# Performance work log

Hardware: AMD Instinct MI355X
Metric: run time of the kernel (lower is better)

The kernel has to match this reference:

```python
import jax, jax.numpy as jnp
import numpy as np

N_EMBD = 1024
HEAD_SIZE = 128
B, T = 8, 4096


def setup_inputs() -> dict:
    key = jax.random.key(0)
    ks = jax.random.split(key, 7)
    s = 1.0 / np.sqrt(N_EMBD)
    return {
        "x": jax.random.normal(ks[0], (B, T, N_EMBD), dtype=jnp.float32),
        "Wq": jax.random.uniform(ks[1], (N_EMBD, HEAD_SIZE), jnp.float32, -s, s),
        "bq": jax.random.uniform(ks[2], (HEAD_SIZE,), jnp.float32, -s, s),
        "Wk": jax.random.uniform(ks[3], (N_EMBD, HEAD_SIZE), jnp.float32, -s, s),
        "bk": jax.random.uniform(ks[4], (HEAD_SIZE,), jnp.float32, -s, s),
        "Wv": jax.random.uniform(ks[5], (N_EMBD, HEAD_SIZE), jnp.float32, -s, s),
        "bv": jax.random.uniform(ks[6], (HEAD_SIZE,), jnp.float32, -s, s),
    }


def reference(x, Wq, bq, Wk, bk, Wv, bv):
    # q,k,v: [B,T,H]
    q = x @ Wq + bq
    k = x @ Wk + bk
    v = x @ Wv + bv
    scale = HEAD_SIZE ** -0.5
    att = jnp.einsum("bth,bsh->bts", q, k) * scale  # [B,T,T]
    t = x.shape[1]
    causal = jnp.tril(jnp.ones((t, t), dtype=bool))
    att = jnp.where(causal, att, -jnp.inf)
    att = jax.nn.softmax(att, axis=-1)
    # dropout with p=0.0 is identity (eval-mode equivalent)
    out = jnp.einsum("bts,bsh->bth", att, v)  # [B,T,H]
    return out
```

## Files before the change

### kernel.cpp

```cpp
#include <hip/hip_runtime.h>
#include <hip/hip_bf16.h>
#include <stdint.h>

#define BATCH 8
#define SEQ   4096
#define EMB   1024
#define HD    128
#define NROWS 32768

typedef __attribute__((ext_vector_type(8))) short short8;
typedef __attribute__((ext_vector_type(4))) float f32x4;

__device__ inline unsigned short f2bf(float f) {
    union { float f; unsigned int u; } c; c.f = f;
    unsigned int u = c.u;
    unsigned int r = (u + 0x7fffu + ((u >> 16) & 1u)) >> 16;
    return (unsigned short)r;
}
__device__ inline float bf2f(unsigned short u) {
    union { unsigned int i; float f; } c; c.i = ((unsigned int)u) << 16; return c.f;
}
__device__ inline unsigned int pkbf(float a, float b) {
    __hip_bfloat162 h = __float22bfloat162_rn(make_float2(a, b));
    union { __hip_bfloat162 h; unsigned int u; } c; c.h = h; return c.u;
}

#define GLDS16(gp, lp) __builtin_amdgcn_global_load_lds( \
    (const __attribute__((address_space(1))) void*)(gp), \
    (__attribute__((address_space(3))) void*)(lp), 16, 0, 0)

__global__ __launch_bounds__(256) void prep_kernel(
    const float* __restrict__ Wq, const float* __restrict__ bq,
    const float* __restrict__ Wk, const float* __restrict__ bk,
    const float* __restrict__ Wv, const float* __restrict__ bv,
    unsigned short* __restrict__ wt, float* __restrict__ biasc)
{
    const int n = blockIdx.x;
    const int sel = n >> 7, h = n & 127;
    const float* W = (sel == 0) ? Wq : (sel == 1) ? Wk : Wv;
    const int tid = threadIdx.x;
    const int k0 = tid * 4;
    union { unsigned short us[4]; uint2 v; } pk;
#pragma unroll
    for (int u = 0; u < 4; ++u) pk.us[u] = f2bf(W[(size_t)(k0 + u) * HD + h]);
    *(uint2*)&wt[(size_t)n * EMB + k0] = pk.v;
    if (tid == 0) {
        const float* bp = (sel == 0) ? bq : (sel == 1) ? bk : bv;
        biasc[n] = bp[h];
    }
}

__global__ __launch_bounds__(768, 3) void gemm_qkv(
    const float* __restrict__ x, const unsigned short* __restrict__ wt,
    const float* __restrict__ biasc,
    unsigned short* __restrict__ q, unsigned short* __restrict__ kOut,
    unsigned short* __restrict__ vt)
{
    const int m0  = blockIdx.x * 128;
    const int tid = threadIdx.x;
    const int wave = tid >> 6, lane = tid & 63;
    const int quad = lane >> 4, l15 = lane & 15;
    const int wm = (wave >= 6) ? 1 : 0;
    const int wn = wave - wm * 6;

    __shared__ __align__(16) unsigned short As[2][128][40];
    __shared__ __align__(16) unsigned short Bs[2][12288];

    f32x4 acc[4][4];
#pragma unroll
    for (int i = 0; i < 4; ++i)
#pragma unroll
        for (int j = 0; j < 4; ++j) acc[i][j] = (f32x4){0.f, 0.f, 0.f, 0.f};

    const int aactive = (tid < 512);
    const int arow = tid >> 3, akc = (tid & 7) * 4;
    float4 aR0, aR1;

#define LOAD_A(kt)                                                          \
    if (aactive) {                                                          \
        aR0 = *(const float4*)(x + (size_t)(m0 + arow) * EMB + (kt) * 32 + akc);        \
        aR1 = *(const float4*)(x + (size_t)(m0 + arow + 64) * EMB + (kt) * 32 + akc);   \
    }
#define WRITE_A(buf)                                                        \
    if (aactive) {                                                          \
        union { unsigned short us[4]; uint2 v; } p0, p1;                    \
        p0.us[0] = f2bf(aR0.x); p0.us[1] = f2bf(aR0.y);                     \
        p0.us[2] = f2bf(aR0.z); p0.us[3] = f2bf(aR0.w);                     \
        *(uint2*)&As[buf][arow][akc] = p0.v;                                \
        p1.us[0] = f2bf(aR1.x); p1.us[1] = f2bf(aR1.y);                     \
        p1.us[2] = f2bf(aR1.z); p1.us[3] = f2bf(aR1.w);                     \
        *(uint2*)&As[buf][arow + 64][akc] = p1.v;                           \
    }
#define STAGE_B(kt, buf)                                                    \
    {                                                                       \
        _Pragma("unroll")                                                   \
        for (int g = 0; g < 2; ++g) {                                       \
            int s0 = (g * 12 + wave) * 64;                                  \
            int s  = s0 + lane;                                             \
            int n  = s >> 2, c = (s & 3) ^ (n & 3);                         \
            GLDS16(wt + (size_t)n * EMB + (kt) * 32 + c * 8,                \
                   &Bs[buf][s0 * 8]);                                       \
        }                                                                   \
    }

    LOAD_A(0); STAGE_B(0, 0); WRITE_A(0);
    int cur = 0;

    for (int kt = 0; kt < 32; ++kt) {
        __syncthreads();
        if (kt < 31) { LOAD_A(kt + 1); STAGE_B(kt + 1, cur ^ 1); }
        short8 af[4], bw[4];
#pragma unroll
        for (int mj = 0; mj < 4; ++mj)
            af[mj] = *(const short8*)&As[cur][wm * 64 + mj * 16 + l15][quad * 8];
#pragma unroll
        for (int ni = 0; ni < 4; ++ni) {
            int n = wn * 64 + ni * 16 + l15;
            bw[ni] = *(const short8*)&Bs[cur][n * 32 + ((quad ^ (n & 3)) << 3)];
        }
#pragma unroll
        for (int ni = 0; ni < 4; ++ni)
#pragma unroll
            for (int mj = 0; mj < 4; ++mj)
                acc[ni][mj] = __builtin_amdgcn_mfma_f32_16x16x32_bf16(
                    bw[ni], af[mj], acc[ni][mj], 0, 0, 0);
        if (kt < 31) WRITE_A(cur ^ 1);
        cur ^= 1;
    }

    const float qscale = 0.08838834764831845f * 1.4426950408889634f;
    const int bb = m0 >> 12;
    const int t0 = m0 & 4095;
    const int mrow0 = m0 + wm * 64;
    const int tl0   = t0 + wm * 64;
#pragma unroll
    for (int ni = 0; ni < 4; ++ni) {
        int colbase = wn * 64 + ni * 16;
        int sel = colbase >> 7;
        int c0 = colbase + quad * 4;
        float4 bv4 = *(const float4*)&biasc[c0];
#pragma unroll
        for (int mj = 0; mj < 4; ++mj) {
            int m = mrow0 + mj * 16 + l15;
            if (sel == 0) {
                union { unsigned short us[4]; uint2 v; } pk;
#pragma unroll
                for (int j = 0; j < 4; ++j)
                    pk.us[j] = f2bf((acc[ni][mj][j] + ((const float*)&bv4)[j]) * qscale);
                *(uint2*)&q[(size_t)m * HD + (c0 & 127)] = pk.v;
            } else if (sel == 1) {
                union { unsigned short us[4]; uint2 v; } pk;
#pragma unroll
                for (int j = 0; j < 4; ++j)
                    pk.us[j] = f2bf(acc[ni][mj][j] + ((const float*)&bv4)[j]);
                *(uint2*)&kOut[(size_t)m * HD + (c0 & 127)] = pk.v;
            } else {
#pragma unroll
                for (int j = 0; j < 4; ++j) {
                    int h = (c0 & 127) + j;
                    vt[((size_t)(bb * 128 + h)) * SEQ + tl0 + mj * 16 + l15] =
                        f2bf(acc[ni][mj][j] + ((const float*)&bv4)[j]);
                }
            }
        }
    }
#undef LOAD_A
#undef WRITE_A
#undef STAGE_B
}

__global__ __launch_bounds__(256, 2) void attn_kernel(
    const unsigned short* __restrict__ q, const unsigned short* __restrict__ k,
    const unsigned short* __restrict__ vt, float* __restrict__ outA,
    unsigned short* __restrict__ Oh, float2* __restrict__ ml)
{
    const int rank = blockIdx.x;
    int qt, parity;
    if (rank < 256) { parity = 0; qt = 31 - (rank >> 3); }
    else            { parity = 1; qt = (rank - 256) >> 3; }
    const int b = rank & 7;
    const int tid  = threadIdx.x;
    const int wave = tid >> 6, lane = tid & 63;
    const int quad = lane >> 4, l15 = lane & 15;
    const int qrow0 = qt * 128 + wave * 32;
    const size_t qbase = (size_t)b * SEQ;
    const size_t vbase = (size_t)b * HD * SEQ;

    __shared__ __align__(16) unsigned short Ks[2][8192];
    __shared__ __align__(16) unsigned short Vs[2][8192];

#define STAGE_KV(kt_, buf_)                                                  \
    {                                                                        \
        _Pragma("unroll")                                                    \
        for (int g = 0; g < 4; ++g) {                                        \
            int s0 = (g * 4 + wave) * 64;                                    \
            int s  = s0 + lane;                                              \
            int key = s >> 4, c = (s & 15) ^ (key & 15);                     \
            GLDS16(k + (qbase + (kt_) * 64 + key) * HD + c * 8,              \
                   &Ks[buf_][s0 * 8]);                                       \
        }                                                                    \
        _Pragma("unroll")                                                    \
        for (int g = 0; g < 4; ++g) {                                        \
            int s0 = (g * 4 + wave) * 64;                                    \
            int s  = s0 + lane;                                              \
            int h = s >> 3, c = (s & 7) ^ (h & 7);                           \
            GLDS16(vt + vbase + (size_t)h * SEQ + (kt_) * 64 + c * 8,        \
                   &Vs[buf_][s0 * 8]);                                       \
        }                                                                    \
    }

    short8 qf[2][4];
#pragma unroll
    for (int mi = 0; mi < 2; ++mi)
#pragma unroll
        for (int kh = 0; kh < 4; ++kh)
            qf[mi][kh] = *(const short8*)(q + (qbase + qrow0 + mi * 16 + l15) * HD + kh * 32 + quad * 8);

    f32x4 o[2][8];
#pragma unroll
    for (int mi = 0; mi < 2; ++mi)
#pragma unroll
        for (int hi = 0; hi < 8; ++hi) o[mi][hi] = (f32x4){0.f, 0.f, 0.f, 0.f};
    float m_r[2] = {-1e30f, -1e30f};
    float l_r[2] = {0.f, 0.f};

    const int bpa0 = (l15 + 16 * ((2 * quad) & 3)) * 4;
    const int bpa1 = (l15 + 16 * ((2 * quad + 1) & 3)) * 4;

    const int niter = qt + 1;
    STAGE_KV(parity, 0);
    int cur = 0;

    for (int i = 0; i < niter; ++i) {
        const int kt = parity + 2 * i;
        const int key0 = kt * 64;
        __syncthreads();
        if (i + 1 < niter) STAGE_KV(kt + 2, cur ^ 1);

        f32x4 s[2][4];
#pragma unroll
        for (int mi = 0; mi < 2; ++mi)
#pragma unroll
            for (int ni = 0; ni < 4; ++ni) s[mi][ni] = (f32x4){0.f, 0.f, 0.f, 0.f};
#pragma unroll
        for (int kh = 0; kh < 4; ++kh) {
#pragma unroll
            for (int ni = 0; ni < 4; ++ni) {
                short8 kf = *(const short8*)&Ks[cur][(ni * 16 + l15) * 128 + (((kh * 4 + quad) ^ l15) << 3)];
                s[0][ni] = __builtin_amdgcn_mfma_f32_16x16x32_bf16(kf, qf[0][kh], s[0][ni], 0, 0, 0);
                s[1][ni] = __builtin_amdgcn_mfma_f32_16x16x32_bf16(kf, qf[1][kh], s[1][ni], 0, 0, 0);
            }
        }
        if (key0 + 63 > qrow0) {
#pragma unroll
            for (int mi = 0; mi < 2; ++mi)
#pragma unroll
                for (int ni = 0; ni < 4; ++ni)
#pragma unroll
                    for (int j = 0; j < 4; ++j) {
                        int key = key0 + ni * 16 + quad * 4 + j;
                        int t   = qrow0 + mi * 16 + l15;
                        if (key > t) s[mi][ni][j] = -1e30f;
                    }
        }
        unsigned int pk[2][4][2];
#pragma unroll
        for (int mi = 0; mi < 2; ++mi) {
            float mx = -1e30f;
#pragma unroll
            for (int ni = 0; ni < 4; ++ni)
#pragma unroll
                for (int j = 0; j < 4; ++j) mx = fmaxf(mx, s[mi][ni][j]);
            mx = fmaxf(mx, __shfl_xor(mx, 16));
            mx = fmaxf(mx, __shfl_xor(mx, 32));
            if (!__all(mx - m_r[mi] <= 8.0f)) {
                float mnew = fmaxf(m_r[mi], mx);
                float alpha = __builtin_amdgcn_exp2f(m_r[mi] - mnew);
                m_r[mi] = mnew;
                l_r[mi] *= alpha;
#pragma unroll
                for (int hi = 0; hi < 8; ++hi) o[mi][hi] *= alpha;
            }
            const float mcur = m_r[mi];
            float rs = 0.f;
#pragma unroll
            for (int ni = 0; ni < 4; ++ni) {
                float p0 = __builtin_amdgcn_exp2f(s[mi][ni][0] - mcur);
                float p1 = __builtin_amdgcn_exp2f(s[mi][ni][1] - mcur);
                float p2 = __builtin_amdgcn_exp2f(s[mi][ni][2] - mcur);
                float p3 = __builtin_amdgcn_exp2f(s[mi][ni][3] - mcur);
                rs += (p0 + p1) + (p2 + p3);
                pk[mi][ni][0] = pkbf(p0, p1);
                pk[mi][ni][1] = pkbf(p2, p3);
            }
            rs += __shfl_xor(rs, 16);
            rs += __shfl_xor(rs, 32);
            l_r[mi] += rs;
        }
        short8 pT[2][2];
#pragma unroll
        for (int mi = 0; mi < 2; ++mi)
#pragma unroll
            for (int sk = 0; sk < 2; ++sk) {
                union { unsigned int u[4]; short8 s8; } pt;
                int lo = 2 * sk, hi_ = 2 * sk + 1;
                unsigned int a0 = (unsigned)__builtin_amdgcn_ds_bpermute(bpa0, (int)pk[mi][lo][0]);
                unsigned int b0 = (unsigned)__builtin_amdgcn_ds_bpermute(bpa0, (int)pk[mi][hi_][0]);
                pt.u[0] = (quad < 2) ? a0 : b0;
                unsigned int a1 = (unsigned)__builtin_amdgcn_ds_bpermute(bpa0, (int)pk[mi][lo][1]);
                unsigned int b1 = (unsigned)__builtin_amdgcn_ds_bpermute(bpa0, (int)pk[mi][hi_][1]);
                pt.u[1] = (quad < 2) ? a1 : b1;
                unsigned int a2 = (unsigned)__builtin_amdgcn_ds_bpermute(bpa1, (int)pk[mi][lo][0]);
                unsigned int b2 = (unsigned)__builtin_amdgcn_ds_bpermute(bpa1, (int)pk[mi][hi_][0]);
                pt.u[2] = (quad < 2) ? a2 : b2;
                unsigned int a3 = (unsigned)__builtin_amdgcn_ds_bpermute(bpa1, (int)pk[mi][lo][1]);
                unsigned int b3 = (unsigned)__builtin_amdgcn_ds_bpermute(bpa1, (int)pk[mi][hi_][1]);
                pt.u[3] = (quad < 2) ? a3 : b3;
                pT[mi][sk] = pt.s8;
            }
#pragma unroll
        for (int sk = 0; sk < 2; ++sk)
#pragma unroll
            for (int hi = 0; hi < 8; ++hi) {
                short8 vf = *(const short8*)&Vs[cur][(hi * 16 + l15) * 64 + (((sk * 4 + quad) ^ (l15 & 7)) << 3)];
                o[0][hi] = __builtin_amdgcn_mfma_f32_16x16x32_bf16(vf, pT[0][sk], o[0][hi], 0, 0, 0);
                o[1][hi] = __builtin_amdgcn_mfma_f32_16x16x32_bf16(vf, pT[1][sk], o[1][hi], 0, 0, 0);
            }
        cur ^= 1;
    }

#pragma unroll
    for (int mi = 0; mi < 2; ++mi) {
        size_t rowg = qbase + qrow0 + mi * 16 + l15;
        if (quad == 0) ml[(size_t)parity * NROWS + rowg] = make_float2(m_r[mi], l_r[mi]);
#pragma unroll
        for (int hi = 0; hi < 8; ++hi) {
            if (parity == 0) {
                *(f32x4*)&outA[rowg * HD + hi * 16 + quad * 4] = o[mi][hi];
            } else {
                union { unsigned short us[4]; uint2 v; } pw;
#pragma unroll
                for (int j = 0; j < 4; ++j) pw.us[j] = f2bf(o[mi][hi][j]);
                *(uint2*)&Oh[rowg * HD + hi * 16 + quad * 4] = pw.v;
            }
        }
    }
#undef STAGE_KV
}

__global__ __launch_bounds__(256) void merge_kernel(
    float* __restrict__ out, const unsigned short* __restrict__ Oh,
    const float2* __restrict__ ml)
{
    int idx = blockIdx.x * 256 + threadIdx.x;
    int row = idx >> 5;
    int hc  = (idx & 31) << 2;
    float2 a = ml[row];
    float2 c = ml[NROWS + row];
    float M  = fmaxf(a.x, c.x);
    float w0 = __builtin_amdgcn_exp2f(a.x - M);
    float w1 = __builtin_amdgcn_exp2f(c.x - M);
    float inv = 1.0f / (w0 * a.y + w1 * c.y);
    f32x4 o0 = *(const f32x4*)&out[(size_t)row * HD + hc];
    union { unsigned short us[4]; uint2 v; } pv;
    pv.v = *(const uint2*)&Oh[(size_t)row * HD + hc];
    f32x4 r;
#pragma unroll
    for (int j = 0; j < 4; ++j)
        r[j] = (w0 * o0[j] + w1 * bf2f(pv.us[j])) * inv;
    *(f32x4*)&out[(size_t)row * HD + hc] = r;
}

extern "C" void kernel_launch(void* const* d_in, const int* in_sizes, int n_in,
                              void* d_out, int out_size, void* d_ws, size_t ws_size,
                              hipStream_t stream) {
    const float* x  = (const float*)d_in[0];
    const float* Wq = (const float*)d_in[1];
    const float* bq = (const float*)d_in[2];
    const float* Wk = (const float*)d_in[3];
    const float* bk = (const float*)d_in[4];
    const float* Wv = (const float*)d_in[5];
    const float* bv = (const float*)d_in[6];
    float* out = (float*)d_out;

    unsigned short* wt    = (unsigned short*)d_ws;
    float*          biasc = (float*)((char*)d_ws + 786432);
    unsigned short* qb    = (unsigned short*)((char*)d_ws + 787968);
    unsigned short* kb    = qb  + (size_t)NROWS * HD;
    unsigned short* vtb   = kb  + (size_t)NROWS * HD;
    unsigned short* Oh    = vtb + (size_t)NROWS * HD;
    float2*         ml    = (float2*)((char*)d_ws + 787968 + 4ull * NROWS * HD * 2);

    prep_kernel<<<dim3(384), 256, 0, stream>>>(Wq, bq, Wk, bk, Wv, bv, wt, biasc);
    gemm_qkv<<<dim3(256), 768, 0, stream>>>(x, wt, biasc, qb, kb, vtb);
    attn_kernel<<<dim3(512), 256, 0, stream>>>(qb, kb, vtb, out, Oh, ml);
    merge_kernel<<<dim3(NROWS * 32 / 256), 256, 0, stream>>>(out, Oh, ml);
}
```

Baseline: 313.0 us.

## Stream-K balance causal attention work units across blocks with multi-segment merge

```diff
diff --git a/kernel.cpp b/kernel.cpp
--- a/kernel.cpp
+++ b/kernel.cpp
@@ -28,6 +28,25 @@
 #define GLDS16(gp, lp) __builtin_amdgcn_global_load_lds( \
     (const __attribute__((address_space(1))) void*)(gp), \
     (__attribute__((address_space(3))) void*)(lp), 16, 0, 0)
+
+__device__ inline void decomp(int it, int& b, int& qt, int& kv) {
+    b = it / 1056;
+    int r = it - b * 1056;
+    int q = (int)((__builtin_sqrtf(4.0f * (float)r + 1.0f) - 1.0f) * 0.5f);
+    while ((q + 1) * (q + 2) <= r) ++q;
+    while (q * (q + 1) > r) --q;
+    qt = q;
+    kv = r - q * (q + 1);
+}
+__device__ inline int chunk_of(int I) {
+    return (I < 4352) ? (I / 17) : (256 + ((I - 4352) >> 4));
+}
+__device__ inline int base1(int qt) {
+    if (qt < 8)  return qt;
+    if (qt < 16) return 8 + 2 * (qt - 8);
+    if (qt < 24) return 24 + 3 * (qt - 16);
+    return 48 + 4 * (qt - 24);
+}
 
 __global__ __launch_bounds__(256) void prep_kernel(
     const float* __restrict__ Wq, const float* __restrict__ bq,
@@ -171,77 +190,105 @@
 
 __global__ __launch_bounds__(256, 2) void attn_kernel(
     const unsigned short* __restrict__ q, const unsigned short* __restrict__ k,
-    const unsigned short* __restrict__ vt, float* __restrict__ outA,
-    unsigned short* __restrict__ Oh, float2* __restrict__ ml)
+    const unsigned short* __restrict__ vt, float* __restrict__ out,
+    float* __restrict__ Oseg, float2* __restrict__ ml)
 {
-    const int rank = blockIdx.x;
-    int qt, parity;
-    if (rank < 256) { parity = 0; qt = 31 - (rank >> 3); }
-    else            { parity = 1; qt = (rank - 256) >> 3; }
-    const int b = rank & 7;
+    const int rank  = blockIdx.x;
+    const int start = (rank < 256) ? 17 * rank : 4352 + ((rank - 256) << 4);
+    const int iend  = start + ((rank < 256) ? 17 : 16);
+
     const int tid  = threadIdx.x;
     const int wave = tid >> 6, lane = tid & 63;
     const int quad = lane >> 4, l15 = lane & 15;
-    const int qrow0 = qt * 128 + wave * 32;
-    const size_t qbase = (size_t)b * SEQ;
-    const size_t vbase = (size_t)b * HD * SEQ;
 
     __shared__ __align__(16) unsigned short Ks[2][8192];
     __shared__ __align__(16) unsigned short Vs[2][8192];
 
-#define STAGE_KV(kt_, buf_)                                                  \
+    const int bpa0 = (l15 + 16 * ((2 * quad) & 3)) * 4;
+    const int bpa1 = (l15 + 16 * ((2 * quad + 1) & 3)) * 4;
+
+#define STAGE_KV(b_, kv_, buf_)                                              \
     {                                                                        \
+        const size_t kb0 = (size_t)(b_) * SEQ + (kv_) * 64;                  \
+        const size_t vb0 = (size_t)(b_) * HD * SEQ + (kv_) * 64;             \
         _Pragma("unroll")                                                    \
         for (int g = 0; g < 4; ++g) {                                        \
             int s0 = (g * 4 + wave) * 64;                                    \
             int s  = s0 + lane;                                              \
             int key = s >> 4, c = (s & 15) ^ (key & 15);                     \
-            GLDS16(k + (qbase + (kt_) * 64 + key) * HD + c * 8,              \
-                   &Ks[buf_][s0 * 8]);                                       \
+            GLDS16(k + (kb0 + key) * HD + c * 8, &Ks[buf_][s0 * 8]);         \
         }                                                                    \
         _Pragma("unroll")                                                    \
         for (int g = 0; g < 4; ++g) {                                        \
             int s0 = (g * 4 + wave) * 64;                                    \
             int s  = s0 + lane;                                              \
             int h = s >> 3, c = (s & 7) ^ (h & 7);                           \
-            GLDS16(vt + vbase + (size_t)h * SEQ + (kt_) * 64 + c * 8,        \
-                   &Vs[buf_][s0 * 8]);                                       \
+            GLDS16(vt + vb0 + (size_t)h * SEQ + c * 8, &Vs[buf_][s0 * 8]);   \
         }                                                                    \
     }
 
+    int b, qt, kv;
+    decomp(start, b, qt, kv);
+
     short8 qf[2][4];
-#pragma unroll
-    for (int mi = 0; mi < 2; ++mi)
-#pragma unroll
-        for (int kh = 0; kh < 4; ++kh)
-            qf[mi][kh] = *(const short8*)(q + (qbase + qrow0 + mi * 16 + l15) * HD + kh * 32 + quad * 8);
-
-    f32x4 o[2][8];
-#pragma unroll
-    for (int mi = 0; mi < 2; ++mi)
-#pragma unroll
-        for (int hi = 0; hi < 8; ++hi) o[mi][hi] = (f32x4){0.f, 0.f, 0.f, 0.f};
-    float m_r[2] = {-1e30f, -1e30f};
-    float l_r[2] = {0.f, 0.f};
-
-    const int bpa0 = (l15 + 16 * ((2 * quad) & 3)) * 4;
-    const int bpa1 = (l15 + 16 * ((2 * quad + 1) & 3)) * 4;
-
-    const int niter = qt + 1;
-    STAGE_KV(parity, 0);
+    f32x4  o[2][8];
+    float  m_r[2], l_r[2];
+    int    qrow0 = 0;
+
+#define CTX_INIT(b_, q_)                                                     \
+    {                                                                        \
+        qrow0 = (q_) * 128 + wave * 32;                                      \
+        const size_t qoff = (size_t)(b_) * SEQ + qrow0;                      \
+        _Pragma("unroll")                                                    \
+        for (int mi = 0; mi < 2; ++mi)                                       \
+            _Pragma("unroll")                                                \
+            for (int kh = 0; kh < 4; ++kh)                                   \
+                qf[mi][kh] = *(const short8*)(q + (qoff + mi * 16 + l15) * HD + kh * 32 + quad * 8); \
+        _Pragma("unroll")                                                    \
+        for (int mi = 0; mi < 2; ++mi) {                                     \
+            _Pragma("unroll")                                                \
+            for (int hi = 0; hi < 8; ++hi) o[mi][hi] = (f32x4){0.f, 0.f, 0.f, 0.f}; \
+            m_r[mi] = -1e30f; l_r[mi] = 0.f;                                 \
+        }                                                                    \
+    }
+
+#define CTX_FLUSH()                                                          \
+    {                                                                        \
+        const int I0 = b * 1056 + qt * (qt + 1);                             \
+        const int j  = rank - chunk_of(I0);                                  \
+        const int rr = wave * 32;                                            \
+        float* obase;                                                        \
+        if (j == 0) obase = out + ((size_t)b * SEQ + qrow0) * HD;            \
+        else obase = Oseg + ((size_t)(b * 80 + base1(qt) + j - 1) * 128 + rr) * HD; \
+        const size_t mlb = ((size_t)(b * 32 + qt) * 5 + j) * 128 + rr;       \
+        _Pragma("unroll")                                                    \
+        for (int mi = 0; mi < 2; ++mi) {                                     \
+            if (quad == 0) ml[mlb + mi * 16 + l15] = make_float2(m_r[mi], l_r[mi]); \
+            _Pragma("unroll")                                                \
+            for (int hi = 0; hi < 8; ++hi)                                   \
+                *(f32x4*)&obase[(size_t)(mi * 16 + l15) * HD + hi * 16 + quad * 4] = o[mi][hi]; \
+        }                                                                    \
+    }
+
+    STAGE_KV(b, kv, 0);
+    CTX_INIT(b, qt);
     int cur = 0;
 
-    for (int i = 0; i < niter; ++i) {
-        const int kt = parity + 2 * i;
-        const int key0 = kt * 64;
+    for (int it = start; it < iend; ++it) {
+        int b2 = 0, qt2 = 0, kv2 = 0;
+        const bool more = (it + 1 < iend);
+        if (more) decomp(it + 1, b2, qt2, kv2);
+
         __syncthreads();
-        if (i + 1 < niter) STAGE_KV(kt + 2, cur ^ 1);
-
+        if (more) STAGE_KV(b2, kv2, cur ^ 1);
+
+        const int key0 = kv * 64;
         f32x4 s[2][4];
 #pragma unroll
         for (int mi = 0; mi < 2; ++mi)
 #pragma unroll
             for (int ni = 0; ni < 4; ++ni) s[mi][ni] = (f32x4){0.f, 0.f, 0.f, 0.f};
+        __builtin_amdgcn_s_setprio(1);
 #pragma unroll
         for (int kh = 0; kh < 4; ++kh) {
 #pragma unroll
@@ -251,6 +298,7 @@
                 s[1][ni] = __builtin_amdgcn_mfma_f32_16x16x32_bf16(kf, qf[1][kh], s[1][ni], 0, 0, 0);
             }
         }
+        __builtin_amdgcn_s_setprio(0);
         if (key0 + 63 > qrow0) {
 #pragma unroll
             for (int mi = 0; mi < 2; ++mi)
@@ -318,6 +366,7 @@
                 pt.u[3] = (quad < 2) ? a3 : b3;
                 pT[mi][sk] = pt.s8;
             }
+        __builtin_amdgcn_s_setprio(1);
 #pragma unroll
         for (int sk = 0; sk < 2; ++sk)
 #pragma unroll
@@ -326,49 +375,53 @@
                 o[0][hi] = __builtin_amdgcn_mfma_f32_16x16x32_bf16(vf, pT[0][sk], o[0][hi], 0, 0, 0);
                 o[1][hi] = __builtin_amdgcn_mfma_f32_16x16x32_bf16(vf, pT[1][sk], o[1][hi], 0, 0, 0);
             }
+        __builtin_amdgcn_s_setprio(0);
+
+        if (kv == 2 * qt + 1 || !more) {
+            CTX_FLUSH();
+            if (more && kv == 2 * qt + 1) CTX_INIT(b2, qt2);
+        }
+        b = b2; qt = qt2; kv = kv2;
         cur ^= 1;
     }
-
-#pragma unroll
-    for (int mi = 0; mi < 2; ++mi) {
-        size_t rowg = qbase + qrow0 + mi * 16 + l15;
-        if (quad == 0) ml[(size_t)parity * NROWS + rowg] = make_float2(m_r[mi], l_r[mi]);
-#pragma unroll
-        for (int hi = 0; hi < 8; ++hi) {
-            if (parity == 0) {
-                *(f32x4*)&outA[rowg * HD + hi * 16 + quad * 4] = o[mi][hi];
-            } else {
-                union { unsigned short us[4]; uint2 v; } pw;
-#pragma unroll
-                for (int j = 0; j < 4; ++j) pw.us[j] = f2bf(o[mi][hi][j]);
-                *(uint2*)&Oh[rowg * HD + hi * 16 + quad * 4] = pw.v;
-            }
-        }
-    }
 #undef STAGE_KV
+#undef CTX_INIT
+#undef CTX_FLUSH
 }
 
 __global__ __launch_bounds__(256) void merge_kernel(
-    float* __restrict__ out, const unsigned short* __restrict__ Oh,
+    float* __restrict__ out, const float* __restrict__ Oseg,
     const float2* __restrict__ ml)
 {
     int idx = blockIdx.x * 256 + threadIdx.x;
     int row = idx >> 5;
     int hc  = (idx & 31) << 2;
-    float2 a = ml[row];
-    float2 c = ml[NROWS + row];
-    float M  = fmaxf(a.x, c.x);
-    float w0 = __builtin_amdgcn_exp2f(a.x - M);
-    float w1 = __builtin_amdgcn_exp2f(c.x - M);
-    float inv = 1.0f / (w0 * a.y + w1 * c.y);
-    f32x4 o0 = *(const f32x4*)&out[(size_t)row * HD + hc];
-    union { unsigned short us[4]; uint2 v; } pv;
-    pv.v = *(const uint2*)&Oh[(size_t)row * HD + hc];
-    f32x4 r;
-#pragma unroll
-    for (int j = 0; j < 4; ++j)
-        r[j] = (w0 * o0[j] + w1 * bf2f(pv.us[j])) * inv;
-    *(f32x4*)&out[(size_t)row * HD + hc] = r;
+    int b = row >> 12, t = row & 4095, qt = t >> 7, rr = t & 127;
+    int I0  = b * 1056 + qt * (qt + 1);
+    int nkv = 2 * (qt + 1);
+    int c_lo = chunk_of(I0);
+    int c_hi = chunk_of(I0 + nkv - 1);
+    int nseg = c_hi - c_lo + 1;
+
+    const float2* mlp = ml + ((size_t)(b * 32 + qt) * 5) * 128 + rr;
+    float2 s0 = mlp[0];
+    float M = s0.x;
+    for (int j = 1; j < nseg; ++j) M = fmaxf(M, mlp[(size_t)j * 128].x);
+
+    float w0 = __builtin_amdgcn_exp2f(s0.x - M);
+    float L  = w0 * s0.y;
+    f32x4 a = *(const f32x4*)&out[(size_t)row * HD + hc];
+    a = a * w0;
+    for (int j = 1; j < nseg; ++j) {
+        float2 mj = mlp[(size_t)j * 128];
+        float w = __builtin_amdgcn_exp2f(mj.x - M);
+        L += w * mj.y;
+        const float* sp = Oseg + ((size_t)(b * 80 + base1(qt) + j - 1) * 128 + rr) * HD + hc;
+        f32x4 sv = *(const f32x4*)sp;
+        a = a + sv * w;
+    }
+    float inv = 1.0f / L;
+    *(f32x4*)&out[(size_t)row * HD + hc] = a * inv;
 }
 
 extern "C" void kernel_launch(void* const* d_in, const int* in_sizes, int n_in,
@@ -388,11 +441,11 @@
     unsigned short* qb    = (unsigned short*)((char*)d_ws + 787968);
     unsigned short* kb    = qb  + (size_t)NROWS * HD;
     unsigned short* vtb   = kb  + (size_t)NROWS * HD;
-    unsigned short* Oh    = vtb + (size_t)NROWS * HD;
-    float2*         ml    = (float2*)((char*)d_ws + 787968 + 4ull * NROWS * HD * 2);
+    float*          Oseg  = (float*)((char*)d_ws + 787968 + 3ull * NROWS * HD * 2);
+    float2*         mlseg = (float2*)((char*)Oseg + 640ull * 128 * HD * 4);
 
     prep_kernel<<<dim3(384), 256, 0, stream>>>(Wq, bq, Wk, bk, Wv, bv, wt, biasc);
     gemm_qkv<<<dim3(256), 768, 0, stream>>>(x, wt, biasc, qb, kb, vtb);
-    attn_kernel<<<dim3(512), 256, 0, stream>>>(qb, kb, vtb, out, Oh, ml);
-    merge_kernel<<<dim3(NROWS * 32 / 256), 256, 0, stream>>>(out, Oh, ml);
-}
+    attn_kernel<<<dim3(512), 256, 0, stream>>>(qb, kb, vtb, out, Oseg, mlseg);
+    merge_kernel<<<dim3(NROWS * 32 / 256), 256, 0, stream>>>(out, Oseg, mlseg);
+}
```

After: 316.8 us. Within noise of the previous version (+1.2%).
